# Kernel optimization log

Measured on AMD Instinct MI355X. Metric: run time of the kernel, lower is better.

## Reference

```python
import jax, jax.numpy as jnp
import numpy as np

B, N1, N2 = 8, 2048, 2048
K1D, K2D, V1D, V2D, AD = 256, 256, 256, 256, 128


def setup_inputs() -> dict:
    key = jax.random.key(0)
    ks = jax.random.split(key, 8)
    scale1 = 1.0 / np.sqrt(K1D)
    scale2 = 1.0 / np.sqrt(K2D)
    return {
        "k1": jax.random.normal(ks[0], (B, N1, K1D), jnp.float32),
        "k2": jax.random.normal(ks[1], (B, N2, K2D), jnp.float32),
        "v1": jax.random.normal(ks[2], (B, N1, V1D), jnp.float32),
        "v2": jax.random.normal(ks[3], (B, N2, V2D), jnp.float32),
        "W1": jax.random.uniform(ks[4], (K1D, AD), jnp.float32, -scale1, scale1),
        "b1": jax.random.uniform(ks[5], (AD,), jnp.float32, -scale1, scale1),
        "W2": jax.random.uniform(ks[6], (K2D, AD), jnp.float32, -scale2, scale2),
        "b2": jax.random.uniform(ks[7], (AD,), jnp.float32, -scale2, scale2),
    }


def reference(k1, k2, v1, v2, W1, b1, W2, b2):
    k1p = k1 @ W1 + b1                      # [B, N1, A]
    k2p = k2 @ W2 + b2                      # [B, N2, A]
    score = jnp.einsum("bnd,bmd->bnm", k1p, k2p)   # [B, N1, N2]
    w1 = jax.nn.softmax(score, axis=1)      # softmax over N1 == softmax(score^T, -1)^T
    w2 = jax.nn.softmax(score, axis=-1)     # [B, N1, N2]
    o1 = jnp.einsum("bnm,bnd->bmd", w1, v1)  # [B, N2, V1D]
    o2 = jnp.einsum("bnm,bmd->bnd", w2, v2)  # [B, N1, V2D]
    return (o2, o1)
```

## Files before the change

kernel.cpp:

```cpp
#include <hip/hip_runtime.h>
#include <hip/hip_bf16.h>

#define B_  8
#define N_  2048
#define KD_ 256
#define AD_ 128
#define VD_ 256

using s16x8 = __attribute__((ext_vector_type(8))) short;
using f16x8 = __attribute__((ext_vector_type(8))) _Float16;
using h2    = __attribute__((ext_vector_type(2))) __fp16;
using f32x4 = __attribute__((ext_vector_type(4))) float;

__device__ __forceinline__ f32x4 mfma16(s16x8 a, s16x8 b, f32x4 c) {
  return __builtin_amdgcn_mfma_f32_16x16x32_f16(
      __builtin_bit_cast(f16x8, a), __builtin_bit_cast(f16x8, b), c, 0, 0, 0);
}
__device__ __forceinline__ s16x8 cvt8(const float* __restrict__ p) {
  union { s16x8 v; h2 h[4]; } u;
  f32x4 a = *(const f32x4*)p;
  f32x4 bq = *(const f32x4*)(p + 4);
  u.h[0] = __builtin_amdgcn_cvt_pkrtz(a[0], a[1]);
  u.h[1] = __builtin_amdgcn_cvt_pkrtz(a[2], a[3]);
  u.h[2] = __builtin_amdgcn_cvt_pkrtz(bq[0], bq[1]);
  u.h[3] = __builtin_amdgcn_cvt_pkrtz(bq[2], bq[3]);
  return u.v;
}

__global__ __launch_bounds__(256) void prep_k(
    const float* __restrict__ k1, const float* __restrict__ k2,
    const float* __restrict__ v1, const float* __restrict__ v2,
    const float* __restrict__ W1, const float* __restrict__ b1f,
    const float* __restrict__ W2, const float* __restrict__ b2f,
    short* __restrict__ q1p, short* __restrict__ q2p,
    short* __restrict__ vt1, short* __restrict__ vt2) {
  __shared__ __align__(16) short sWT[128 * 264];
  const int t  = threadIdx.x;
  const int id = blockIdx.x;

  if (id < 512) {
    const int kt = id & 31, b = (id >> 5) & 7, z = id >> 8;
    const float* src = z ? v2 : v1;
    short*       dst = z ? vt2 : vt1;
    const size_t base = ((size_t)(b * 32 + kt)) * (256 * 64);
    const int w = t >> 6, vchunk = (t >> 4) & 3, l16 = t & 15;
    #pragma unroll
    for (int i = 0; i < 8; i++) {
      float x[8];
      #pragma unroll
      for (int kk = 0; kk < 8; kk++)
        x[kk] = src[((size_t)(b * N_ + kt * 64 + i * 8 + kk)) * VD_ + t];
      union { s16x8 v; h2 h[4]; } u;
      #pragma unroll
      for (int kk = 0; kk < 4; kk++)
        u.h[kk] = __builtin_amdgcn_cvt_pkrtz(x[2 * kk], x[2 * kk + 1]);
      int f = vchunk * 2 + (i >> 2);
      *(s16x8*)&dst[base + (size_t)((w * 8 + f) * 64 + (i & 3) * 16 + l16) * 8] = u.v;
    }
    return;
  }

  const int pid = id - 512;
  const int z = pid >> 8, mb = pid & 255;
  const float* X    = z ? k2 : k1;
  const float* W    = z ? W2 : W1;
  const float* bias = z ? b2f : b1f;
  short*       Y    = z ? q2p : q1p;
  const int m0   = mb * 64;
  const int lane = t & 63, wave = t >> 6, quad = lane >> 4, l16 = lane & 15;

  #pragma unroll
  for (int j = 0; j < 64; j++) {
    int idx = j * 256 + t;
    int n = idx & 127, kh = idx >> 7;
    h2 p = __builtin_amdgcn_cvt_pkrtz(W[(size_t)(2 * kh) * AD_ + n],
                                      W[(size_t)(2 * kh + 1) * AD_ + n]);
    *(h2*)&sWT[n * 264 + kh * 2] = p;
  }
  const float* xrow = &X[(size_t)(m0 + wave * 16 + l16) * KD_];
  s16x8 a[8];
  #pragma unroll
  for (int ks = 0; ks < 8; ks++) a[ks] = cvt8(xrow + ks * 32 + quad * 8);
  __syncthreads();

  f32x4 acc[8];
  #pragma unroll
  for (int nt = 0; nt < 8; nt++) acc[nt] = (f32x4){0.f, 0.f, 0.f, 0.f};
  #pragma unroll
  for (int ks = 0; ks < 8; ks++) {
    #pragma unroll
    for (int nt = 0; nt < 8; nt++) {
      s16x8 bf = *(const s16x8*)&sWT[(nt * 16 + l16) * 264 + ks * 32 + quad * 8];
      acc[nt] = mfma16(a[ks], bf, acc[nt]);
    }
  }
  #pragma unroll
  for (int nt = 0; nt < 8; nt++) {
    float bv = bias[nt * 16 + l16];
    #pragma unroll
    for (int r = 0; r < 4; r++) {
      int row = m0 + wave * 16 + quad * 4 + r;
      _Float16 h = (_Float16)(acc[nt][r] + bv);
      Y[(size_t)row * AD_ + nt * 16 + l16] = *reinterpret_cast<short*>(&h);
    }
  }
}

__global__ __launch_bounds__(256, 2) void attn_k(
    const short* __restrict__ q1p, const short* __restrict__ q2p,
    const short* __restrict__ vt1, const short* __restrict__ vt2,
    float* __restrict__ out) {
  __shared__ __align__(16) short sK[2][64 * 136];
  __shared__ __align__(16) short sP[2][4][16 * 64];
  __shared__ __align__(16) float sAl[2][68];

  const int t    = threadIdx.x;
  const int lane = t & 63, wave = t >> 6, quad = lane >> 4, l16 = lane & 15;
  const int id   = blockIdx.x;
  const int xcd  = id & 7, seq = id >> 3;
  const int bp   = xcd * 2 + (seq >> 5);
  const int qb   = seq & 31;
  const int b    = bp & 7, pass = bp >> 3;
  const int q0   = qb * 64;
  const short* Q  = pass ? q2p : q1p;
  const short* K  = pass ? q1p : q2p;
  const short* Vt = pass ? vt1 : vt2;
  float* O = out + (size_t)pass * ((size_t)B_ * N_ * VD_);

  const short* kp = K + (size_t)(b * N_) * AD_ + (size_t)(t >> 4) * AD_ + (t & 15) * 8;
  const short* vp = Vt + (size_t)b * 32 * (256 * 64) + wave * 4096 + lane * 8;

  s16x8 qf[4];
  #pragma unroll
  for (int ks = 0; ks < 4; ks++)
    qf[ks] = *(const s16x8*)&Q[((size_t)(b * N_ + q0 + wave * 16 + l16)) * AD_ +
                               ks * 32 + quad * 8];

  float m_i = -1e30f, l_i = 0.f;
  f32x4 acc[16];
  #pragma unroll
  for (int c0 = 0; c0 < 16; c0++) acc[c0] = (f32x4){0.f, 0.f, 0.f, 0.f};

  s16x8 pk[4], pv[8];
  auto loadK = [&]() {
    #pragma unroll
    for (int i = 0; i < 4; i++)
      pk[i] = *(const s16x8*)(kp + i * 16 * AD_);
    kp += 64 * AD_;
  };
  auto loadV = [&]() {
    #pragma unroll
    for (int f = 0; f < 8; f++)
      pv[f] = *(const s16x8*)(vp + f * 512);
    vp += 256 * 64;
  };
  auto storeK = [&](int cb) {
    #pragma unroll
    for (int i = 0; i < 4; i++) {
      int chunk = i * 256 + t, row = chunk >> 4, c8 = chunk & 15;
      *(s16x8*)&sK[cb][row * 136 + c8 * 8] = pk[i];
    }
  };

  loadK();
  storeK(0);
  loadK();
  loadV();
  __syncthreads();

  int c = 0;
  for (int kt = 0; kt < 32; kt++) {
    f32x4 st[4];
    #pragma unroll
    for (int nt = 0; nt < 4; nt++) st[nt] = (f32x4){0.f, 0.f, 0.f, 0.f};
    __builtin_amdgcn_s_setprio(1);
    #pragma unroll
    for (int ks = 0; ks < 4; ks++) {
      #pragma unroll
      for (int nt = 0; nt < 4; nt++) {
        s16x8 kf = *(const s16x8*)&sK[c][(nt * 16 + l16) * 136 + ks * 32 + quad * 8];
        st[nt] = mfma16(kf, qf[ks], st[nt]);
      }
    }
    __builtin_amdgcn_s_setprio(0);

    float mt = st[0][0];
    #pragma unroll
    for (int nt = 0; nt < 4; nt++) {
      #pragma unroll
      for (int r = 0; r < 4; r++) mt = fmaxf(mt, st[nt][r]);
    }
    mt = fmaxf(mt, __shfl_xor(mt, 16));
    mt = fmaxf(mt, __shfl_xor(mt, 32));

    float alpha = 1.f;
    bool  resc  = !__all(mt - m_i <= 8.f);
    if (resc) {
      float mn = fmaxf(m_i, mt);
      alpha = __expf(m_i - mn);
      l_i *= alpha;
      m_i  = mn;
    }

    f32x4 psv = (f32x4){0.f, 0.f, 0.f, 0.f};
    #pragma unroll
    for (int nt = 0; nt < 4; nt++) {
      #pragma unroll
      for (int r = 0; r < 4; r++) {
        float p = __expf(st[nt][r] - m_i);
        st[nt][r] = p;
        psv[r] += p;
      }
    }
    float sum = (psv[0] + psv[1]) + (psv[2] + psv[3]);
    sum += __shfl_xor(sum, 16);
    sum += __shfl_xor(sum, 32);
    l_i += sum;

    #pragma unroll
    for (int nt = 0; nt < 4; nt++) {
      union { h2 h[2]; uint2 u; } wu;
      wu.h[0] = __builtin_amdgcn_cvt_pkrtz(st[nt][0], st[nt][1]);
      wu.h[1] = __builtin_amdgcn_cvt_pkrtz(st[nt][2], st[nt][3]);
      int cp = (nt * 4 + quad) ^ ((l16 & 7) << 1);
      *(uint2*)&sP[c][wave][l16 * 64 + cp * 4] = wu.u;
    }
    if (quad == 0) sAl[c][wave * 16 + l16] = alpha;
    if (lane == 0) sAl[c][64 + wave] = resc ? 1.f : 0.f;

    if (kt + 1 < 32) storeK(1 - c);

    __syncthreads();

    if (kt + 2 < 32) loadK();

    f32x4 fl = *(const f32x4*)&sAl[c][64];
    if (fl[0] + fl[1] + fl[2] + fl[3] != 0.f) {
      #pragma unroll
      for (int m = 0; m < 4; m++) {
        f32x4 aR = *(const f32x4*)&sAl[c][m * 16 + quad * 4];
        #pragma unroll
        for (int v = 0; v < 4; v++) {
          #pragma unroll
          for (int r = 0; r < 4; r++) acc[m * 4 + v][r] *= aR[r];
        }
      }
    }

    __builtin_amdgcn_s_setprio(1);
    #pragma unroll
    for (int m = 0; m < 4; m++) {
      #pragma unroll
      for (int ks2 = 0; ks2 < 2; ks2++) {
        int cp = (ks2 * 8 + quad * 2) ^ ((l16 & 7) << 1);
        s16x8 af = *(const s16x8*)&sP[c][m][l16 * 64 + cp * 4];
        #pragma unroll
        for (int v = 0; v < 4; v++)
          acc[m * 4 + v] = mfma16(af, pv[v * 2 + ks2], acc[m * 4 + v]);
      }
    }
    __builtin_amdgcn_s_setprio(0);

    if (kt + 1 < 32) loadV();
    c ^= 1;
  }

  if (quad == 0) sAl[0][wave * 16 + l16] = l_i;
  __syncthreads();
  #pragma unroll
  for (int m = 0; m < 4; m++) {
    f32x4 lv = *(const f32x4*)&sAl[0][m * 16 + quad * 4];
    #pragma unroll
    for (int r = 0; r < 4; r++) {
      float inv = 1.f / lv[r];
      int row = q0 + m * 16 + quad * 4 + r;
      #pragma unroll
      for (int v = 0; v < 4; v++)
        O[((size_t)(b * N_ + row)) * VD_ + wave * 64 + v * 16 + l16] =
            acc[m * 4 + v][r] * inv;
    }
  }
}

extern "C" void kernel_launch(void* const* d_in, const int* in_sizes, int n_in,
                              void* d_out, int out_size, void* d_ws, size_t ws_size,
                              hipStream_t stream) {
  const float* k1 = (const float*)d_in[0];
  const float* k2 = (const float*)d_in[1];
  const float* v1 = (const float*)d_in[2];
  const float* v2 = (const float*)d_in[3];
  const float* W1 = (const float*)d_in[4];
  const float* b1 = (const float*)d_in[5];
  const float* W2 = (const float*)d_in[6];
  const float* b2 = (const float*)d_in[7];

  short* ws  = (short*)d_ws;
  short* q1p = ws;
  short* q2p = q1p + (size_t)16384 * 128;
  short* vt1 = q2p + (size_t)16384 * 128;
  short* vt2 = vt1 + (size_t)B_ * 32 * 256 * 64;
  float* out = (float*)d_out;

  prep_k<<<dim3(1024), dim3(256), 0, stream>>>(k1, k2, v1, v2, W1, b1, W2, b2,
                                               q1p, q2p, vt1, vt2);
  attn_k<<<dim3(512), dim3(256), 0, stream>>>(q1p, q2p, vt1, vt2, out);
}
```

Before: 181.6 us.

## Fuse projection and attention into one persistent kernel with grid barrier

Merges the prep kernel (projection and V transpose) and the attention kernel into a single launch of 512 blocks, separated by an atomic-counter grid-wide barrier. Each block now does one V-tile transpose and one projection tile before attending. log2(e) is folded into the projection weights so the softmax can use exp2f. Row-sum reduction across lanes is moved out of the inner loop to the epilogue. This removes a kernel launch boundary and tail gap but adds a spin barrier that requires all 512 blocks to be co-resident, plus a memset launch.

```diff
diff --git a/kernel.cpp b/kernel.cpp
--- a/kernel.cpp
+++ b/kernel.cpp
@@ -6,6 +6,7 @@
 #define KD_ 256
 #define AD_ 128
 #define VD_ 256
+#define SQL2E 1.2011224087864498f
 
 using s16x8 = __attribute__((ext_vector_type(8))) short;
 using f16x8 = __attribute__((ext_vector_type(8))) _Float16;
@@ -15,6 +16,10 @@
 __device__ __forceinline__ f32x4 mfma16(s16x8 a, s16x8 b, f32x4 c) {
   return __builtin_amdgcn_mfma_f32_16x16x32_f16(
       __builtin_bit_cast(f16x8, a), __builtin_bit_cast(f16x8, b), c, 0, 0, 0);
+}
+__device__ __forceinline__ short f2h(float f) {
+  _Float16 h = (_Float16)f;
+  return *reinterpret_cast<short*>(&h);
 }
 __device__ __forceinline__ s16x8 cvt8(const float* __restrict__ p) {
   union { s16x8 v; h2 h[4]; } u;
@@ -27,257 +32,264 @@
   return u.v;
 }
 
-__global__ __launch_bounds__(256) void prep_k(
+__global__ __launch_bounds__(256, 2) void fused_k(
     const float* __restrict__ k1, const float* __restrict__ k2,
     const float* __restrict__ v1, const float* __restrict__ v2,
     const float* __restrict__ W1, const float* __restrict__ b1f,
     const float* __restrict__ W2, const float* __restrict__ b2f,
     short* __restrict__ q1p, short* __restrict__ q2p,
-    short* __restrict__ vt1, short* __restrict__ vt2) {
-  __shared__ __align__(16) short sWT[128 * 264];
-  const int t  = threadIdx.x;
-  const int id = blockIdx.x;
-
-  if (id < 512) {
-    const int kt = id & 31, b = (id >> 5) & 7, z = id >> 8;
-    const float* src = z ? v2 : v1;
-    short*       dst = z ? vt2 : vt1;
-    const size_t base = ((size_t)(b * 32 + kt)) * (256 * 64);
-    const int w = t >> 6, vchunk = (t >> 4) & 3, l16 = t & 15;
+    short* __restrict__ vt1, short* __restrict__ vt2,
+    float* __restrict__ out, unsigned* cnt) {
+  extern __shared__ f32x4 smemv[];
+  char* smem = (char*)smemv;
+
+  const int t   = threadIdx.x;
+  const int id  = blockIdx.x;
+  const int xcd = id & 7, seq = id >> 3;
+  const int bp  = xcd * 2 + (seq >> 5);
+  const int pb  = bp & 7;
+  const int ph  = bp >> 3;
+  const int j32 = seq & 31;
+
+  {
+    const int a = ph ^ 1;
+    const float* src = a ? v2 : v1;
+    short* dst = a ? vt2 : vt1;
+    const size_t base = ((size_t)(pb * 32 + j32)) * (256 * 64);
+    const int w = t >> 6, vch = (t >> 4) & 3, l16 = t & 15;
     #pragma unroll
     for (int i = 0; i < 8; i++) {
       float x[8];
       #pragma unroll
       for (int kk = 0; kk < 8; kk++)
-        x[kk] = src[((size_t)(b * N_ + kt * 64 + i * 8 + kk)) * VD_ + t];
+        x[kk] = src[((size_t)(pb * N_ + j32 * 64 + i * 8 + kk)) * VD_ + t];
       union { s16x8 v; h2 h[4]; } u;
       #pragma unroll
       for (int kk = 0; kk < 4; kk++)
         u.h[kk] = __builtin_amdgcn_cvt_pkrtz(x[2 * kk], x[2 * kk + 1]);
-      int f = vchunk * 2 + (i >> 2);
+      int f = vch * 2 + (i >> 2);
       *(s16x8*)&dst[base + (size_t)((w * 8 + f) * 64 + (i & 3) * 16 + l16) * 8] = u.v;
     }
-    return;
   }
-
-  const int pid = id - 512;
-  const int z = pid >> 8, mb = pid & 255;
-  const float* X    = z ? k2 : k1;
-  const float* W    = z ? W2 : W1;
-  const float* bias = z ? b2f : b1f;
-  short*       Y    = z ? q2p : q1p;
-  const int m0   = mb * 64;
-  const int lane = t & 63, wave = t >> 6, quad = lane >> 4, l16 = lane & 15;
-
-  #pragma unroll
-  for (int j = 0; j < 64; j++) {
-    int idx = j * 256 + t;
-    int n = idx & 127, kh = idx >> 7;
-    h2 p = __builtin_amdgcn_cvt_pkrtz(W[(size_t)(2 * kh) * AD_ + n],
-                                      W[(size_t)(2 * kh + 1) * AD_ + n]);
-    *(h2*)&sWT[n * 264 + kh * 2] = p;
+  {
+    const int z = ph ^ 1;
+    const float* X    = z ? k2 : k1;
+    const float* W    = z ? W2 : W1;
+    const float* bias = z ? b2f : b1f;
+    short*       Y    = z ? q2p : q1p;
+    const int m0 = (pb * 32 + j32) * 64;
+    const int lane = t & 63, wave = t >> 6, quad = lane >> 4, l16 = lane & 15;
+    short* sWT = (short*)smem;
+
+    const float* xrow = &X[(size_t)(m0 + wave * 16 + l16) * KD_];
+    s16x8 a8[8];
+    #pragma unroll
+    for (int ks = 0; ks < 8; ks++) a8[ks] = cvt8(xrow + ks * 32 + quad * 8);
+    f32x4 acc8[8];
+    #pragma unroll
+    for (int nt = 0; nt < 8; nt++) acc8[nt] = (f32x4){0.f, 0.f, 0.f, 0.f};
+    #pragma unroll
+    for (int h = 0; h < 2; h++) {
+      #pragma unroll
+      for (int j = 0; j < 32; j++) {
+        int idx = j * 256 + t, n = idx & 127, kh = idx >> 7;
+        const float* wp = &W[(size_t)(h * 128 + kh * 2) * AD_ + n];
+        h2 p = __builtin_amdgcn_cvt_pkrtz(wp[0] * SQL2E, wp[AD_] * SQL2E);
+        *(h2*)&sWT[n * 136 + kh * 2] = p;
+      }
+      __syncthreads();
+      #pragma unroll
+      for (int ks = 0; ks < 4; ks++) {
+        #pragma unroll
+        for (int nt = 0; nt < 8; nt++) {
+          s16x8 bf = *(const s16x8*)&sWT[(nt * 16 + l16) * 136 + ks * 32 + quad * 8];
+          acc8[nt] = mfma16(a8[h * 4 + ks], bf, acc8[nt]);
+        }
+      }
+      __syncthreads();
+    }
+    #pragma unroll
+    for (int nt = 0; nt < 8; nt++) {
+      float bv = bias[nt * 16 + l16] * SQL2E;
+      #pragma unroll
+      for (int r = 0; r < 4; r++) {
+        int row = m0 + wave * 16 + quad * 4 + r;
+        Y[(size_t)row * AD_ + nt * 16 + l16] = f2h(acc8[nt][r] + bv);
+      }
+    }
   }
-  const float* xrow = &X[(size_t)(m0 + wave * 16 + l16) * KD_];
-  s16x8 a[8];
-  #pragma unroll
-  for (int ks = 0; ks < 8; ks++) a[ks] = cvt8(xrow + ks * 32 + quad * 8);
+
   __syncthreads();
-
-  f32x4 acc[8];
-  #pragma unroll
-  for (int nt = 0; nt < 8; nt++) acc[nt] = (f32x4){0.f, 0.f, 0.f, 0.f};
-  #pragma unroll
-  for (int ks = 0; ks < 8; ks++) {
-    #pragma unroll
-    for (int nt = 0; nt < 8; nt++) {
-      s16x8 bf = *(const s16x8*)&sWT[(nt * 16 + l16) * 264 + ks * 32 + quad * 8];
-      acc[nt] = mfma16(a[ks], bf, acc[nt]);
-    }
+  if (t == 0) {
+    __threadfence();
+    unsigned ticket = atomicAdd(cnt, 1u) + 1u;
+    unsigned target = (ticket + 511u) & ~511u;
+    while (__hip_atomic_load(cnt, __ATOMIC_RELAXED, __HIP_MEMORY_SCOPE_AGENT) < target)
+      __builtin_amdgcn_s_sleep(8);
+    __threadfence();
   }
-  #pragma unroll
-  for (int nt = 0; nt < 8; nt++) {
-    float bv = bias[nt * 16 + l16];
-    #pragma unroll
-    for (int r = 0; r < 4; r++) {
-      int row = m0 + wave * 16 + quad * 4 + r;
-      _Float16 h = (_Float16)(acc[nt][r] + bv);
-      Y[(size_t)row * AD_ + nt * 16 + l16] = *reinterpret_cast<short*>(&h);
-    }
-  }
-}
-
-__global__ __launch_bounds__(256, 2) void attn_k(
-    const short* __restrict__ q1p, const short* __restrict__ q2p,
-    const short* __restrict__ vt1, const short* __restrict__ vt2,
-    float* __restrict__ out) {
-  __shared__ __align__(16) short sK[2][64 * 136];
-  __shared__ __align__(16) short sP[2][4][16 * 64];
-  __shared__ __align__(16) float sAl[2][68];
-
-  const int t    = threadIdx.x;
-  const int lane = t & 63, wave = t >> 6, quad = lane >> 4, l16 = lane & 15;
-  const int id   = blockIdx.x;
-  const int xcd  = id & 7, seq = id >> 3;
-  const int bp   = xcd * 2 + (seq >> 5);
-  const int qb   = seq & 31;
-  const int b    = bp & 7, pass = bp >> 3;
-  const int q0   = qb * 64;
-  const short* Q  = pass ? q2p : q1p;
-  const short* K  = pass ? q1p : q2p;
-  const short* Vt = pass ? vt1 : vt2;
-  float* O = out + (size_t)pass * ((size_t)B_ * N_ * VD_);
-
-  const short* kp = K + (size_t)(b * N_) * AD_ + (size_t)(t >> 4) * AD_ + (t & 15) * 8;
-  const short* vp = Vt + (size_t)b * 32 * (256 * 64) + wave * 4096 + lane * 8;
-
-  s16x8 qf[4];
-  #pragma unroll
-  for (int ks = 0; ks < 4; ks++)
-    qf[ks] = *(const s16x8*)&Q[((size_t)(b * N_ + q0 + wave * 16 + l16)) * AD_ +
-                               ks * 32 + quad * 8];
-
-  float m_i = -1e30f, l_i = 0.f;
-  f32x4 acc[16];
-  #pragma unroll
-  for (int c0 = 0; c0 < 16; c0++) acc[c0] = (f32x4){0.f, 0.f, 0.f, 0.f};
-
-  s16x8 pk[4], pv[8];
-  auto loadK = [&]() {
-    #pragma unroll
-    for (int i = 0; i < 4; i++)
-      pk[i] = *(const s16x8*)(kp + i * 16 * AD_);
-    kp += 64 * AD_;
-  };
-  auto loadV = [&]() {
-    #pragma unroll
-    for (int f = 0; f < 8; f++)
-      pv[f] = *(const s16x8*)(vp + f * 512);
-    vp += 256 * 64;
-  };
-  auto storeK = [&](int cb) {
-    #pragma unroll
-    for (int i = 0; i < 4; i++) {
-      int chunk = i * 256 + t, row = chunk >> 4, c8 = chunk & 15;
-      *(s16x8*)&sK[cb][row * 136 + c8 * 8] = pk[i];
-    }
-  };
-
-  loadK();
-  storeK(0);
-  loadK();
-  loadV();
   __syncthreads();
 
-  int c = 0;
-  for (int kt = 0; kt < 32; kt++) {
-    f32x4 st[4];
-    #pragma unroll
-    for (int nt = 0; nt < 4; nt++) st[nt] = (f32x4){0.f, 0.f, 0.f, 0.f};
-    __builtin_amdgcn_s_setprio(1);
-    #pragma unroll
-    for (int ks = 0; ks < 4; ks++) {
+  {
+    const int lane = t & 63, wave = t >> 6, quad = lane >> 4, l16 = lane & 15;
+    const int b = pb, pass = ph, q0 = j32 * 64;
+    const short* Q  = pass ? q2p : q1p;
+    const short* K  = pass ? q1p : q2p;
+    const short* Vt = pass ? vt1 : vt2;
+    float* O = out + (size_t)pass * ((size_t)B_ * N_ * VD_);
+
+    short* sKb  = (short*)smem;
+    short* sPb  = (short*)(smem + 34816);
+    float* sAlb = (float*)(smem + 34816 + 16384);
+
+    const short* kp = K + (size_t)(b * N_) * AD_ + (size_t)(t >> 4) * AD_ + (t & 15) * 8;
+    const short* vp = Vt + (size_t)b * 32 * (256 * 64) + wave * 4096 + lane * 8;
+
+    s16x8 qf[4];
+    #pragma unroll
+    for (int ks = 0; ks < 4; ks++)
+      qf[ks] = *(const s16x8*)&Q[((size_t)(b * N_ + q0 + wave * 16 + l16)) * AD_ +
+                                 ks * 32 + quad * 8];
+
+    float m_i = -1e30f, l_i = 0.f;
+    f32x4 acc[16];
+    #pragma unroll
+    for (int c0 = 0; c0 < 16; c0++) acc[c0] = (f32x4){0.f, 0.f, 0.f, 0.f};
+
+    s16x8 pk[4], pv[8];
+    auto loadK = [&]() {
+      #pragma unroll
+      for (int i = 0; i < 4; i++) pk[i] = *(const s16x8*)(kp + i * 16 * AD_);
+      kp += 64 * AD_;
+    };
+    auto loadV = [&]() {
+      #pragma unroll
+      for (int f = 0; f < 8; f++) pv[f] = *(const s16x8*)(vp + f * 512);
+      vp += 256 * 64;
+    };
+    auto storeK = [&](int cb) {
+      short* d = sKb + cb * (64 * 136);
+      #pragma unroll
+      for (int i = 0; i < 4; i++) {
+        int chunk = i * 256 + t, row = chunk >> 4, c8 = chunk & 15;
+        *(s16x8*)&d[row * 136 + c8 * 8] = pk[i];
+      }
+    };
+
+    loadK(); storeK(0); loadK(); loadV();
+    __syncthreads();
+
+    int c = 0;
+    for (int kt = 0; kt < 32; kt++) {
+      const short* sk = sKb + c * (64 * 136);
+      f32x4 st[4];
+      #pragma unroll
+      for (int nt = 0; nt < 4; nt++) st[nt] = (f32x4){0.f, 0.f, 0.f, 0.f};
+      __builtin_amdgcn_s_setprio(1);
+      #pragma unroll
+      for (int ks = 0; ks < 4; ks++) {
+        #pragma unroll
+        for (int nt = 0; nt < 4; nt++) {
+          s16x8 kf = *(const s16x8*)&sk[(nt * 16 + l16) * 136 + ks * 32 + quad * 8];
+          st[nt] = mfma16(kf, qf[ks], st[nt]);
+        }
+      }
+      __builtin_amdgcn_s_setprio(0);
+
+      float c0 = fmaxf(fmaxf(st[0][0], st[1][0]), fmaxf(st[2][0], st[3][0]));
+      float c1 = fmaxf(fmaxf(st[0][1], st[1][1]), fmaxf(st[2][1], st[3][1]));
+      float c2 = fmaxf(fmaxf(st[0][2], st[1][2]), fmaxf(st[2][2], st[3][2]));
+      float c3 = fmaxf(fmaxf(st[0][3], st[1][3]), fmaxf(st[2][3], st[3][3]));
+      float mt = fmaxf(fmaxf(c0, c1), fmaxf(c2, c3));
+      mt = fmaxf(mt, __shfl_xor(mt, 16));
+      mt = fmaxf(mt, __shfl_xor(mt, 32));
+
+      float alpha = 1.f;
+      bool  resc  = !__all(mt - m_i <= 8.f);
+      if (resc) {
+        float mn = fmaxf(m_i, mt);
+        alpha = exp2f(m_i - mn);
+        l_i *= alpha;
+        m_i  = mn;
+      }
+
+      f32x4 psv = (f32x4){0.f, 0.f, 0.f, 0.f};
       #pragma unroll
       for (int nt = 0; nt < 4; nt++) {
-        s16x8 kf = *(const s16x8*)&sK[c][(nt * 16 + l16) * 136 + ks * 32 + quad * 8];
-        st[nt] = mfma16(kf, qf[ks], st[nt]);
-      }
-    }
-    __builtin_amdgcn_s_setprio(0);
-
-    float mt = st[0][0];
-    #pragma unroll
-    for (int nt = 0; nt < 4; nt++) {
-      #pragma unroll
-      for (int r = 0; r < 4; r++) mt = fmaxf(mt, st[nt][r]);
-    }
-    mt = fmaxf(mt, __shfl_xor(mt, 16));
-    mt = fmaxf(mt, __shfl_xor(mt, 32));
-
-    float alpha = 1.f;
-    bool  resc  = !__all(mt - m_i <= 8.f);
-    if (resc) {
-      float mn = fmaxf(m_i, mt);
-      alpha = __expf(m_i - mn);
-      l_i *= alpha;
-      m_i  = mn;
-    }
-
-    f32x4 psv = (f32x4){0.f, 0.f, 0.f, 0.f};
-    #pragma unroll
-    for (int nt = 0; nt < 4; nt++) {
+        #pragma unroll
+        for (int r = 0; r < 4; r++) {
+          float p = exp2f(st[nt][r] - m_i);
+          st[nt][r] = p;
+          psv[r] += p;
+        }
+      }
+      l_i += (psv[0] + psv[1]) + (psv[2] + psv[3]);
+
+      float* sAl = sAlb + c * 68;
+      short* sPw = sPb + (c * 4 + wave) * 1024;
+      #pragma unroll
+      for (int nt = 0; nt < 4; nt++) {
+        union { h2 h[2]; uint2 u; } wu;
+        wu.h[0] = __builtin_amdgcn_cvt_pkrtz(st[nt][0], st[nt][1]);
+        wu.h[1] = __builtin_amdgcn_cvt_pkrtz(st[nt][2], st[nt][3]);
+        int cp = (nt * 4 + quad) ^ ((l16 & 7) << 1);
+        *(uint2*)&sPw[l16 * 64 + cp * 4] = wu.u;
+      }
+      if (quad == 0) sAl[wave * 16 + l16] = alpha;
+      if (lane == 0) sAl[64 + wave] = resc ? 1.f : 0.f;
+
+      if (kt + 1 < 32) storeK(1 - c);
+      __syncthreads();
+      if (kt + 2 < 32) loadK();
+
+      f32x4 fl = *(const f32x4*)&sAl[64];
+      if (fl[0] + fl[1] + fl[2] + fl[3] != 0.f) {
+        #pragma unroll
+        for (int m = 0; m < 4; m++) {
+          f32x4 aR = *(const f32x4*)&sAl[m * 16 + quad * 4];
+          #pragma unroll
+          for (int v = 0; v < 4; v++) {
+            #pragma unroll
+            for (int r = 0; r < 4; r++) acc[m * 4 + v][r] *= aR[r];
+          }
+        }
+      }
+
+      __builtin_amdgcn_s_setprio(1);
+      #pragma unroll
+      for (int m = 0; m < 4; m++) {
+        const short* sPm = sPb + (c * 4 + m) * 1024;
+        #pragma unroll
+        for (int ks2 = 0; ks2 < 2; ks2++) {
+          int cp = (ks2 * 8 + quad * 2) ^ ((l16 & 7) << 1);
+          s16x8 af = *(const s16x8*)&sPm[l16 * 64 + cp * 4];
+          #pragma unroll
+          for (int v = 0; v < 4; v++)
+            acc[m * 4 + v] = mfma16(af, pv[v * 2 + ks2], acc[m * 4 + v]);
+        }
+      }
+      __builtin_amdgcn_s_setprio(0);
+
+      if (kt + 1 < 32) loadV();
+      c ^= 1;
+    }
+
+    float lf = l_i + __shfl_xor(l_i, 16);
+    lf += __shfl_xor(lf, 32);
+    if (quad == 0) sAlb[wave * 16 + l16] = lf;
+    __syncthreads();
+    #pragma unroll
+    for (int m = 0; m < 4; m++) {
+      f32x4 lv = *(const f32x4*)&sAlb[m * 16 + quad * 4];
       #pragma unroll
       for (int r = 0; r < 4; r++) {
-        float p = __expf(st[nt][r] - m_i);
-        st[nt][r] = p;
-        psv[r] += p;
-      }
-    }
-    float sum = (psv[0] + psv[1]) + (psv[2] + psv[3]);
-    sum += __shfl_xor(sum, 16);
-    sum += __shfl_xor(sum, 32);
-    l_i += sum;
-
-    #pragma unroll
-    for (int nt = 0; nt < 4; nt++) {
-      union { h2 h[2]; uint2 u; } wu;
-      wu.h[0] = __builtin_amdgcn_cvt_pkrtz(st[nt][0], st[nt][1]);
-      wu.h[1] = __builtin_amdgcn_cvt_pkrtz(st[nt][2], st[nt][3]);
-      int cp = (nt * 4 + quad) ^ ((l16 & 7) << 1);
-      *(uint2*)&sP[c][wave][l16 * 64 + cp * 4] = wu.u;
-    }
-    if (quad == 0) sAl[c][wave * 16 + l16] = alpha;
-    if (lane == 0) sAl[c][64 + wave] = resc ? 1.f : 0.f;
-
-    if (kt + 1 < 32) storeK(1 - c);
-
-    __syncthreads();
-
-    if (kt + 2 < 32) loadK();
-
-    f32x4 fl = *(const f32x4*)&sAl[c][64];
-    if (fl[0] + fl[1] + fl[2] + fl[3] != 0.f) {
-      #pragma unroll
-      for (int m = 0; m < 4; m++) {
-        f32x4 aR = *(const f32x4*)&sAl[c][m * 16 + quad * 4];
-        #pragma unroll
-        for (int v = 0; v < 4; v++) {
-          #pragma unroll
-          for (int r = 0; r < 4; r++) acc[m * 4 + v][r] *= aR[r];
-        }
-      }
-    }
-
-    __builtin_amdgcn_s_setprio(1);
-    #pragma unroll
-    for (int m = 0; m < 4; m++) {
-      #pragma unroll
-      for (int ks2 = 0; ks2 < 2; ks2++) {
-        int cp = (ks2 * 8 + quad * 2) ^ ((l16 & 7) << 1);
-        s16x8 af = *(const s16x8*)&sP[c][m][l16 * 64 + cp * 4];
+        float inv = 1.f / lv[r];
+        int row = q0 + m * 16 + quad * 4 + r;
         #pragma unroll
         for (int v = 0; v < 4; v++)
-          acc[m * 4 + v] = mfma16(af, pv[v * 2 + ks2], acc[m * 4 + v]);
-      }
-    }
-    __builtin_amdgcn_s_setprio(0);
-
-    if (kt + 1 < 32) loadV();
-    c ^= 1;
-  }
-
-  if (quad == 0) sAl[0][wave * 16 + l16] = l_i;
-  __syncthreads();
-  #pragma unroll
-  for (int m = 0; m < 4; m++) {
-    f32x4 lv = *(const f32x4*)&sAl[0][m * 16 + quad * 4];
-    #pragma unroll
-    for (int r = 0; r < 4; r++) {
-      float inv = 1.f / lv[r];
-      int row = q0 + m * 16 + quad * 4 + r;
-      #pragma unroll
-      for (int v = 0; v < 4; v++)
-        O[((size_t)(b * N_ + row)) * VD_ + wave * 64 + v * 16 + l16] =
-            acc[m * 4 + v][r] * inv;
+          O[((size_t)(b * N_ + row)) * VD_ + wave * 64 + v * 16 + l16] =
+              acc[m * 4 + v][r] * inv;
+      }
     }
   }
 }
@@ -294,14 +306,15 @@
   const float* W2 = (const float*)d_in[6];
   const float* b2 = (const float*)d_in[7];
 
-  short* ws  = (short*)d_ws;
-  short* q1p = ws;
+  unsigned* cnt = (unsigned*)d_ws;
+  short* base = (short*)d_ws + 8;
+  short* q1p = base;
   short* q2p = q1p + (size_t)16384 * 128;
   short* vt1 = q2p + (size_t)16384 * 128;
   short* vt2 = vt1 + (size_t)B_ * 32 * 256 * 64;
   float* out = (float*)d_out;
 
-  prep_k<<<dim3(1024), dim3(256), 0, stream>>>(k1, k2, v1, v2, W1, b1, W2, b2,
-                                               q1p, q2p, vt1, vt2);
-  attn_k<<<dim3(512), dim3(256), 0, stream>>>(q1p, q2p, vt1, vt2, out);
-}
+  hipMemsetAsync(cnt, 0, 4, stream);
+  fused_k<<<dim3(512), dim3(256), 51744, stream>>>(
+      k1, k2, v1, v2, W1, b1, W2, b2, q1p, q2p, vt1, vt2, out, cnt);
+}
```

Measured after the change: 255.8 us. 40.9% more time.

## Software-pipeline QK^T one tile ahead of PV and fold log2e into projections

Applied to the files above, without the earlier changes.

The attention loop is restructured so the QK^T MFMAs and softmax for tile i+1 run in the same iteration as the PV MFMAs for tile i. This lets the matrix and vector work of neighbouring tiles overlap, and with both stages in one loop body there is one barrier per iteration. The projection weights and bias are pre-scaled by sqrt(log2 e), so the softmax can use exp2f directly without an extra multiply. Row-sum cross-lane shuffles are deferred to the end, and K loads are issued one tile further ahead, which costs more registers and more LDS buffer juggling.

```diff
diff --git a/kernel.cpp b/kernel.cpp
--- a/kernel.cpp
+++ b/kernel.cpp
@@ -6,6 +6,7 @@
 #define KD_ 256
 #define AD_ 128
 #define VD_ 256
+#define SQL2E 1.2011224087864498f
 
 using s16x8 = __attribute__((ext_vector_type(8))) short;
 using f16x8 = __attribute__((ext_vector_type(8))) _Float16;
@@ -15,6 +16,10 @@
 __device__ __forceinline__ f32x4 mfma16(s16x8 a, s16x8 b, f32x4 c) {
   return __builtin_amdgcn_mfma_f32_16x16x32_f16(
       __builtin_bit_cast(f16x8, a), __builtin_bit_cast(f16x8, b), c, 0, 0, 0);
+}
+__device__ __forceinline__ short f2h(float f) {
+  _Float16 h = (_Float16)f;
+  return *reinterpret_cast<short*>(&h);
 }
 __device__ __forceinline__ s16x8 cvt8(const float* __restrict__ p) {
   union { s16x8 v; h2 h[4]; } u;
@@ -73,8 +78,8 @@
   for (int j = 0; j < 64; j++) {
     int idx = j * 256 + t;
     int n = idx & 127, kh = idx >> 7;
-    h2 p = __builtin_amdgcn_cvt_pkrtz(W[(size_t)(2 * kh) * AD_ + n],
-                                      W[(size_t)(2 * kh + 1) * AD_ + n]);
+    h2 p = __builtin_amdgcn_cvt_pkrtz(W[(size_t)(2 * kh) * AD_ + n] * SQL2E,
+                                      W[(size_t)(2 * kh + 1) * AD_ + n] * SQL2E);
     *(h2*)&sWT[n * 264 + kh * 2] = p;
   }
   const float* xrow = &X[(size_t)(m0 + wave * 16 + l16) * KD_];
@@ -96,12 +101,11 @@
   }
   #pragma unroll
   for (int nt = 0; nt < 8; nt++) {
-    float bv = bias[nt * 16 + l16];
+    float bv = bias[nt * 16 + l16] * SQL2E;
     #pragma unroll
     for (int r = 0; r < 4; r++) {
       int row = m0 + wave * 16 + quad * 4 + r;
-      _Float16 h = (_Float16)(acc[nt][r] + bv);
-      Y[(size_t)row * AD_ + nt * 16 + l16] = *reinterpret_cast<short*>(&h);
+      Y[(size_t)row * AD_ + nt * 16 + l16] = f2h(acc[nt][r] + bv);
     }
   }
 }
@@ -144,14 +148,12 @@
   s16x8 pk[4], pv[8];
   auto loadK = [&]() {
     #pragma unroll
-    for (int i = 0; i < 4; i++)
-      pk[i] = *(const s16x8*)(kp + i * 16 * AD_);
+    for (int i = 0; i < 4; i++) pk[i] = *(const s16x8*)(kp + i * 16 * AD_);
     kp += 64 * AD_;
   };
   auto loadV = [&]() {
     #pragma unroll
-    for (int f = 0; f < 8; f++)
-      pv[f] = *(const s16x8*)(vp + f * 512);
+    for (int f = 0; f < 8; f++) pv[f] = *(const s16x8*)(vp + f * 512);
     vp += 256 * 64;
   };
   auto storeK = [&](int cb) {
@@ -161,16 +163,7 @@
       *(s16x8*)&sK[cb][row * 136 + c8 * 8] = pk[i];
     }
   };
-
-  loadK();
-  storeK(0);
-  loadK();
-  loadV();
-  __syncthreads();
-
-  int c = 0;
-  for (int kt = 0; kt < 32; kt++) {
-    f32x4 st[4];
+  auto qk = [&](int cb, f32x4* st) {
     #pragma unroll
     for (int nt = 0; nt < 4; nt++) st[nt] = (f32x4){0.f, 0.f, 0.f, 0.f};
     __builtin_amdgcn_s_setprio(1);
@@ -178,61 +171,67 @@
     for (int ks = 0; ks < 4; ks++) {
       #pragma unroll
       for (int nt = 0; nt < 4; nt++) {
-        s16x8 kf = *(const s16x8*)&sK[c][(nt * 16 + l16) * 136 + ks * 32 + quad * 8];
+        s16x8 kf = *(const s16x8*)&sK[cb][(nt * 16 + l16) * 136 + ks * 32 + quad * 8];
         st[nt] = mfma16(kf, qf[ks], st[nt]);
       }
     }
     __builtin_amdgcn_s_setprio(0);
-
-    float mt = st[0][0];
-    #pragma unroll
-    for (int nt = 0; nt < 4; nt++) {
-      #pragma unroll
-      for (int r = 0; r < 4; r++) mt = fmaxf(mt, st[nt][r]);
-    }
+  };
+  auto softmax_store = [&](f32x4* st, int cb) {
+    float c0 = fmaxf(fmaxf(st[0][0], st[1][0]), fmaxf(st[2][0], st[3][0]));
+    float c1 = fmaxf(fmaxf(st[0][1], st[1][1]), fmaxf(st[2][1], st[3][1]));
+    float c2 = fmaxf(fmaxf(st[0][2], st[1][2]), fmaxf(st[2][2], st[3][2]));
+    float c3 = fmaxf(fmaxf(st[0][3], st[1][3]), fmaxf(st[2][3], st[3][3]));
+    float mt = fmaxf(fmaxf(c0, c1), fmaxf(c2, c3));
     mt = fmaxf(mt, __shfl_xor(mt, 16));
     mt = fmaxf(mt, __shfl_xor(mt, 32));
-
     float alpha = 1.f;
     bool  resc  = !__all(mt - m_i <= 8.f);
     if (resc) {
       float mn = fmaxf(m_i, mt);
-      alpha = __expf(m_i - mn);
+      alpha = exp2f(m_i - mn);
       l_i *= alpha;
       m_i  = mn;
     }
-
     f32x4 psv = (f32x4){0.f, 0.f, 0.f, 0.f};
     #pragma unroll
     for (int nt = 0; nt < 4; nt++) {
       #pragma unroll
       for (int r = 0; r < 4; r++) {
-        float p = __expf(st[nt][r] - m_i);
+        float p = exp2f(st[nt][r] - m_i);
         st[nt][r] = p;
         psv[r] += p;
       }
     }
-    float sum = (psv[0] + psv[1]) + (psv[2] + psv[3]);
-    sum += __shfl_xor(sum, 16);
-    sum += __shfl_xor(sum, 32);
-    l_i += sum;
-
+    l_i += (psv[0] + psv[1]) + (psv[2] + psv[3]);
     #pragma unroll
     for (int nt = 0; nt < 4; nt++) {
       union { h2 h[2]; uint2 u; } wu;
       wu.h[0] = __builtin_amdgcn_cvt_pkrtz(st[nt][0], st[nt][1]);
       wu.h[1] = __builtin_amdgcn_cvt_pkrtz(st[nt][2], st[nt][3]);
       int cp = (nt * 4 + quad) ^ ((l16 & 7) << 1);
-      *(uint2*)&sP[c][wave][l16 * 64 + cp * 4] = wu.u;
-    }
-    if (quad == 0) sAl[c][wave * 16 + l16] = alpha;
-    if (lane == 0) sAl[c][64 + wave] = resc ? 1.f : 0.f;
-
-    if (kt + 1 < 32) storeK(1 - c);
-
+      *(uint2*)&sP[cb][wave][l16 * 64 + cp * 4] = wu.u;
+    }
+    if (quad == 0) sAl[cb][wave * 16 + l16] = alpha;
+    if (lane == 0) sAl[cb][64 + wave] = resc ? 1.f : 0.f;
+  };
+
+  loadK(); storeK(0); loadK(); loadV();
+  __syncthreads();
+  {
+    f32x4 st[4];
+    qk(0, st);
+    softmax_store(st, 0);
+  }
+  storeK(1);
+  loadK();
+
+  for (int i = 0; i < 32; i++) {
+    const int c = i & 1;
     __syncthreads();
 
-    if (kt + 2 < 32) loadK();
+    f32x4 st[4];
+    if (i + 1 < 32) qk(1 - c, st);
 
     f32x4 fl = *(const f32x4*)&sAl[c][64];
     if (fl[0] + fl[1] + fl[2] + fl[3] != 0.f) {
@@ -261,11 +260,16 @@
     }
     __builtin_amdgcn_s_setprio(0);
 
-    if (kt + 1 < 32) loadV();
-    c ^= 1;
-  }
-
-  if (quad == 0) sAl[0][wave * 16 + l16] = l_i;
+    if (i + 1 < 32) softmax_store(st, 1 - c);
+
+    if (i + 2 < 32) storeK(c);
+    if (i + 3 < 32) loadK();
+    if (i + 1 < 32) loadV();
+  }
+
+  float lf = l_i + __shfl_xor(l_i, 16);
+  lf += __shfl_xor(lf, 32);
+  if (quad == 0) sAl[0][wave * 16 + l16] = lf;
   __syncthreads();
   #pragma unroll
   for (int m = 0; m < 4; m++) {
```

After: 185.4 us. 2.1% more time.
